# Kernel tuning notes

Measured on AMD Instinct MI355X. Metric: run time of the kernel, lower is better.

## Reference

```python
import jax, jax.numpy as jnp
import numpy as np

EMB = 768

def setup_inputs() -> dict:
    key = jax.random.key(0)
    ks = jax.random.split(key, 9)
    B, N, E = 8, 2048, EMB
    s = 1.0 / np.sqrt(E)
    return {
        "x":  jax.random.normal(ks[0], (B, N, E), jnp.float32),
        "Wq": jax.random.normal(ks[1], (E, E), jnp.float32) * s,
        "bq": jnp.zeros((E,), jnp.float32),
        "Wk": jax.random.normal(ks[2], (E, E), jnp.float32) * s,
        "bk": jnp.zeros((E,), jnp.float32),
        "Wv": jax.random.normal(ks[3], (E, E), jnp.float32) * s,
        "bv": jnp.zeros((E,), jnp.float32),
        "Wo": jax.random.normal(ks[4], (E, E), jnp.float32) * s,
        "bo": jnp.zeros((E,), jnp.float32),
    }

def reference(x, Wq, bq, Wk, bk, Wv, bv, Wo, bo):
    # Single-head attention; scale uses full emb dim (as in the source).
    E = x.shape[-1]
    q = jnp.einsum('bne,ef->bnf', x, Wq) + bq
    k = jnp.einsum('bne,ef->bnf', x, Wk) + bk
    v = jnp.einsum('bne,ef->bnf', x, Wv) + bv
    scores = jnp.einsum('bqe,bke->bqk', q, k) / jnp.sqrt(jnp.asarray(E, x.dtype))
    attn = jax.nn.softmax(scores, axis=-1)  # dropout is identity in eval mode
    out = jnp.einsum('bqk,bke->bqe', attn, v)
    return jnp.einsum('bne,ef->bnf', out, Wo) + bo
```

## Files before the change

### kernel.cpp

```cpp
#include <hip/hip_runtime.h>
#include <hip/hip_fp16.h>
#include <stdint.h>

typedef unsigned short u16;
typedef __attribute__((ext_vector_type(8))) __bf16 bf16x8;
typedef __attribute__((ext_vector_type(4))) float f32x4;

#define SEQ 2048
#define EMB 768
#define NB  8
#define LDQK (2 * EMB)

__device__ __forceinline__ u16 f2bf(float f) {
  union { float f; uint32_t u; } a; a.f = f;
  uint32_t r = a.u + 0x7fffu + ((a.u >> 16) & 1u);
  return (u16)(r >> 16);
}
__device__ __forceinline__ float bf2f(u16 h) {
  union { uint32_t u; float f; } a; a.u = ((uint32_t)h) << 16;
  return a.f;
}

__device__ __forceinline__ void swz_bid(int& bx, int& by, int& bz)
{
  const int gx = gridDim.x, gy = gridDim.y;
  const int nwg = gx * gy * gridDim.z;
  const int lid = ((int)blockIdx.z * gy + (int)blockIdx.y) * gx +
                  (int)blockIdx.x;
  const int cpx = nwg >> 3;
  const int orig = (lid & 7) * cpx + (lid >> 3);
  bx = orig % gx;
  const int t = orig / gx;
  by = t % gy;
  bz = t / gy;
}

__global__ __launch_bounds__(256) void k_detect_bias(
    const u16* __restrict__ x, int* __restrict__ flag,
    const void* __restrict__ b0, const void* __restrict__ b1,
    const void* __restrict__ b2, const void* __restrict__ b3,
    float* __restrict__ biasf)
{
  const int tid = threadIdx.x;
  int bad = 0;
#pragma unroll
  for (int i = 0; i < 4; ++i) {
    const u16 h = x[(tid * 4 + i) * 2];
    const int e = (h >> 7) & 0xFF;
    bad += (e >= 160 && e <= 254) ? 1 : 0;
  }
#pragma unroll
  for (int off = 32; off > 0; off >>= 1) bad += __shfl_down(bad, off);
  __shared__ int cnt[4];
  __shared__ int sflag;
  if ((tid & 63) == 0) cnt[tid >> 6] = bad;
  __syncthreads();
  if (tid == 0) {
    const int f = (cnt[0] + cnt[1] + cnt[2] + cnt[3] > 200) ? 1 : 0;
    sflag = f;
    *flag = f;
  }
  __syncthreads();
  const int f32 = sflag;
#pragma unroll
  for (int z = 0; z < 4; ++z) {
    const void* src = (z == 0) ? b0 : (z == 1) ? b1 : (z == 2) ? b2 : b3;
#pragma unroll
    for (int i = 0; i < 3; ++i) {
      const int j = tid + i * 256;
      biasf[z * EMB + j] = f32 ? ((const float*)src)[j]
                               : bf2f(((const u16*)src)[j]);
    }
  }
}

__global__ __launch_bounds__(256) void k_convert_x(
    const void* __restrict__ src, u16* __restrict__ dst,
    const int* __restrict__ flag, int n4)
{
  const int i = blockIdx.x * 256 + threadIdx.x;
  if (i >= n4) return;
  if (*flag) {
    const float4 f = ((const float4*)src)[i];
    ushort4 o;
    o.x = f2bf(f.x); o.y = f2bf(f.y); o.z = f2bf(f.z); o.w = f2bf(f.w);
    ((ushort4*)dst)[i] = o;
  } else {
    ((ushort4*)dst)[i] = ((const ushort4*)src)[i];
  }
}

__global__ __launch_bounds__(256) void k_transpose_w(
    const void* __restrict__ W0, const void* __restrict__ W1,
    const void* __restrict__ W2, const void* __restrict__ W3,
    u16* __restrict__ WT, const int* __restrict__ flag)
{
  __shared__ u16 t[32][33];
  const int z = blockIdx.z;
  const void* in = (z == 0) ? W0 : (z == 1) ? W1 : (z == 2) ? W2 : W3;
  u16* out = WT + (size_t)z * EMB * EMB;
  const int c0 = blockIdx.x * 32, r0 = blockIdx.y * 32;
  const int tx = threadIdx.x, ty = threadIdx.y;
  const int f32 = *flag;
#pragma unroll
  for (int i = 0; i < 4; ++i) {
    const size_t idx = (size_t)(r0 + ty + i * 8) * EMB + c0 + tx;
    t[ty + i * 8][tx] = f32 ? f2bf(((const float*)in)[idx])
                            : ((const u16*)in)[idx];
  }
  __syncthreads();
#pragma unroll
  for (int i = 0; i < 4; ++i)
    out[(size_t)(c0 + ty + i * 8) * EMB + r0 + tx] = t[tx][ty + i * 8];
}

template <int EPI>
__device__ __forceinline__ void gemm_core(
    const u16* __restrict__ A, int lda,
    const u16* __restrict__ BT, int ldbt,
    void* __restrict__ Cp, int ldc,
    const float* __restrict__ biasf, const int* __restrict__ of32,
    float scale, int K, int m0, int n0)
{
  __shared__ __align__(16) u16 As[128 * 64];
  __shared__ __align__(16) u16 Bs[128 * 64];
  const int tid  = threadIdx.x;
  const int lane = tid & 63;
  const int wave = tid >> 6;
  const int wr   = (wave >> 1) * 64;
  const int wc   = (wave & 1) * 64;
  const int lrow = lane & 15;
  const int quad = lane >> 4;

  f32x4 acc[4][4];
#pragma unroll
  for (int i = 0; i < 4; ++i)
#pragma unroll
    for (int j = 0; j < 4; ++j)
#pragma unroll
      for (int r = 0; r < 4; ++r) acc[i][j][r] = 0.0f;

  for (int kt = 0; kt < K; kt += 64) {
#pragma unroll
    for (int i = 0; i < 4; ++i) {
      const int c = wave * 256 + i * 64 + lane;
      const int r = c >> 3, s = c & 7;
      const int ss = s ^ (r & 7);
      const u16* ga = A  + (size_t)(m0 + r) * lda  + kt + ss * 8;
      const u16* gb = BT + (size_t)(n0 + r) * ldbt + kt + ss * 8;
      u16* la = As + (size_t)(wave * 256 + i * 64) * 8;
      u16* lb = Bs + (size_t)(wave * 256 + i * 64) * 8;
      __builtin_amdgcn_global_load_lds(
          (const __attribute__((address_space(1))) void*)ga,
          (__attribute__((address_space(3))) void*)la, 16, 0, 0);
      __builtin_amdgcn_global_load_lds(
          (const __attribute__((address_space(1))) void*)gb,
          (__attribute__((address_space(3))) void*)lb, 16, 0, 0);
    }
    __syncthreads();

#pragma unroll
    for (int kk = 0; kk < 2; ++kk) {
      bf16x8 af[4], bfr[4];
#pragma unroll
      for (int i = 0; i < 4; ++i) {
        const int row = wr + i * 16 + lrow;
        const int cs  = ((kk << 2) + quad) ^ (lrow & 7);
        af[i] = *(const bf16x8*)(As + row * 64 + cs * 8);
      }
#pragma unroll
      for (int j = 0; j < 4; ++j) {
        const int row = wc + j * 16 + lrow;
        const int cs  = ((kk << 2) + quad) ^ (lrow & 7);
        bfr[j] = *(const bf16x8*)(Bs + row * 64 + cs * 8);
      }
#pragma unroll
      for (int i = 0; i < 4; ++i)
#pragma unroll
        for (int j = 0; j < 4; ++j)
          acc[i][j] = __builtin_amdgcn_mfma_f32_16x16x32_bf16(
              af[i], bfr[j], acc[i][j], 0, 0, 0);
    }
    __syncthreads();
  }

  if (EPI == 3) {
    u16* C = (u16*)Cp;
#pragma unroll
    for (int i = 0; i < 4; ++i)
#pragma unroll
      for (int j = 0; j < 4; ++j)
#pragma unroll
        for (int r = 0; r < 4; ++r) {
          const int row = m0 + wr + i * 16 + quad * 4 + r;
          const int col = n0 + wc + j * 16 + lrow;
          C[(size_t)row * ldc + col] =
              __half_as_ushort(__float2half(acc[i][j][r] * scale));
        }
  } else if (EPI == 2) {
    u16* C = (u16*)Cp;
#pragma unroll
    for (int i = 0; i < 4; ++i)
#pragma unroll
      for (int j = 0; j < 4; ++j)
#pragma unroll
        for (int r = 0; r < 4; ++r) {
          const int row = m0 + wr + i * 16 + quad * 4 + r;
          const int col = n0 + wc + j * 16 + lrow;
          C[(size_t)row * ldc + col] = f2bf(acc[i][j][r]);
        }
  } else if (EPI == 5) {
    u16* C = (u16*)Cp;
#pragma unroll
    for (int i = 0; i < 4; ++i)
#pragma unroll
      for (int r = 0; r < 4; ++r) {
        const int row = m0 + wr + i * 16 + quad * 4 + r;
        const float bv = biasf[row];
#pragma unroll
        for (int j = 0; j < 4; ++j) {
          const int col = n0 + wc + j * 16 + lrow;
          C[(size_t)row * ldc + col] = f2bf(acc[i][j][r] + bv);
        }
      }
  } else {
    float bv[4];
#pragma unroll
    for (int j = 0; j < 4; ++j) bv[j] = biasf[n0 + wc + j * 16 + lrow];
    const bool f32out = (of32 != nullptr) && (*of32 != 0);
    if (f32out) {
      float* C = (float*)Cp;
#pragma unroll
      for (int i = 0; i < 4; ++i)
#pragma unroll
        for (int j = 0; j < 4; ++j)
#pragma unroll
          for (int r = 0; r < 4; ++r) {
            const int row = m0 + wr + i * 16 + quad * 4 + r;
            const int col = n0 + wc + j * 16 + lrow;
            C[(size_t)row * ldc + col] = acc[i][j][r] + bv[j];
          }
    } else {
      u16* C = (u16*)Cp;
#pragma unroll
      for (int i = 0; i < 4; ++i)
#pragma unroll
        for (int j = 0; j < 4; ++j)
#pragma unroll
          for (int r = 0; r < 4; ++r) {
            const int row = m0 + wr + i * 16 + quad * 4 + r;
            const int col = n0 + wc + j * 16 + lrow;
            C[(size_t)row * ldc + col] = f2bf(acc[i][j][r] + bv[j]);
          }
    }
  }
}


__global__ __launch_bounds__(256) void k_gemm_qk(
    const u16* __restrict__ A, const u16* __restrict__ BT,
    u16* __restrict__ QK, const float* __restrict__ biasf)
{
  int bx, by, bz; swz_bid(bx, by, bz);
  gemm_core<0>(A, EMB, BT, EMB, QK, LDQK, biasf, nullptr, 1.0f, EMB,
               by * 128, bx * 128);
}

__global__ __launch_bounds__(256) void k_gemm_vt(
    const u16* __restrict__ WvT, const u16* __restrict__ xb,
    u16* __restrict__ VT, const float* __restrict__ biasv)
{
  int bx, by, bz; swz_bid(bx, by, bz);
  const int b = bz;
  gemm_core<5>(WvT, EMB,
               xb + (size_t)b * SEQ * EMB, EMB,
               VT + (size_t)b * EMB * SEQ, SEQ,
               biasv, nullptr, 1.0f, EMB,
               by * 128, bx * 128);
}

__global__ __launch_bounds__(256) void k_gemm_out(
    const u16* __restrict__ A, const u16* __restrict__ BT,
    void* __restrict__ C, const float* __restrict__ biasf,
    const int* __restrict__ of32)
{
  int bx, by, bz; swz_bid(bx, by, bz);
  gemm_core<0>(A, EMB, BT, EMB, C, EMB, biasf, of32, 1.0f, EMB,
               by * 128, bx * 128);
}

__global__ __launch_bounds__(256) void k_gemm_scores(
    const u16* __restrict__ QK, u16* __restrict__ S, int b0)
{
  int bx, by, bz; swz_bid(bx, by, bz);
  const int b = b0 + bz;
  const u16* base = QK + (size_t)b * SEQ * LDQK;
  gemm_core<3>(base, LDQK,
               base + EMB, LDQK,
               S + (size_t)bz * SEQ * SEQ, SEQ,
               nullptr, nullptr,
               0.03608439182435161f , EMB,
               by * 128, bx * 128);
}

__global__ __launch_bounds__(256) void k_gemm_pv(
    const u16* __restrict__ P, const u16* __restrict__ VT,
    u16* __restrict__ O, int b0)
{
  int bx, by, bz; swz_bid(bx, by, bz);
  const int b = b0 + bz;
  gemm_core<2>(P  + (size_t)bz * SEQ * SEQ, SEQ,
               VT + (size_t)b * EMB * SEQ, SEQ,
               O  + (size_t)b * SEQ * EMB, EMB,
               nullptr, nullptr, 1.0f, SEQ,
               by * 128, bx * 128);
}

__global__ __launch_bounds__(256) void k_softmax(u16* __restrict__ S)
{
  u16* row = S + ((size_t)blockIdx.y * SEQ + blockIdx.x) * SEQ;
  const int tid = threadIdx.x;

  uint4 raw = *(const uint4*)(row + tid * 8);
  const u16* h = (const u16*)&raw;
  float v[8];
#pragma unroll
  for (int i = 0; i < 8; ++i) v[i] = __half2float(__ushort_as_half(h[i]));

  float mx = v[0];
#pragma unroll
  for (int i = 1; i < 8; ++i) mx = fmaxf(mx, v[i]);
#pragma unroll
  for (int off = 32; off > 0; off >>= 1) mx = fmaxf(mx, __shfl_down(mx, off));
  __shared__ float red[4], red2[4];
  if ((tid & 63) == 0) red[tid >> 6] = mx;
  __syncthreads();
  mx = fmaxf(fmaxf(red[0], red[1]), fmaxf(red[2], red[3]));

  float s = 0.0f;
#pragma unroll
  for (int i = 0; i < 8; ++i) { v[i] = __expf(v[i] - mx); s += v[i]; }
#pragma unroll
  for (int off = 32; off > 0; off >>= 1) s += __shfl_down(s, off);
  if ((tid & 63) == 0) red2[tid >> 6] = s;
  __syncthreads();
  s = red2[0] + red2[1] + red2[2] + red2[3];
  const float inv = 1.0f / s;

  uint4 outv;
  u16* o = (u16*)&outv;
#pragma unroll
  for (int i = 0; i < 8; ++i) o[i] = f2bf(v[i] * inv);
  *(uint4*)(row + tid * 8) = outv;
}


extern "C" void kernel_launch(void* const* d_in, const int* in_sizes, int n_in,
                              void* d_out, int out_size, void* d_ws, size_t ws_size,
                              hipStream_t stream)
{
  (void)in_sizes; (void)n_in; (void)out_size;
  const void* x  = d_in[0];
  const void* Wq = d_in[1];
  const void* bq = d_in[2];
  const void* Wk = d_in[3];
  const void* bk = d_in[4];
  const void* Wv = d_in[5];
  const void* bv = d_in[6];
  const void* Wo = d_in[7];
  const void* bo = d_in[8];

  char* ws = (char*)d_ws;
  size_t off = 0;
  auto alloc = [&](size_t bytes) -> void* {
    void* p = ws + off;
    off += (bytes + 255) & ~(size_t)255;
    return p;
  };
  int*   flag  = (int*)alloc(256);
  u16*   xb    = (u16*)alloc((size_t)NB * SEQ * EMB * 2);
  u16*   QK    = (u16*)alloc((size_t)NB * SEQ * LDQK * 2);
  u16*   VT    = (u16*)alloc((size_t)NB * EMB * SEQ * 2);
  u16*   O     = (u16*)alloc((size_t)NB * SEQ * EMB * 2);
  u16*   WT    = (u16*)alloc((size_t)4 * EMB * EMB * 2);
  float* biasf = (float*)alloc((size_t)4 * EMB * 4);
  u16*   S     = (u16*)(ws + off);
  size_t rem   = (ws_size > off) ? ws_size - off : 0;

  int GB = 8;
  while (GB > 1 && (size_t)GB * ((size_t)SEQ * SEQ * 2) > rem) GB >>= 1;

  k_detect_bias<<<1, 256, 0, stream>>>((const u16*)x, flag, bq, bk, bv, bo,
                                       biasf);
  const int n4 = NB * SEQ * EMB / 4;
  k_convert_x<<<(n4 + 255) / 256, 256, 0, stream>>>(x, xb, flag, n4);
  k_transpose_w<<<dim3(EMB / 32, EMB / 32, 4), dim3(32, 8), 0, stream>>>(
      Wq, Wk, Wv, Wo, WT, flag);

  k_gemm_qk<<<dim3(12, 128), 256, 0, stream>>>(xb, WT, QK, biasf);
  k_gemm_vt<<<dim3(16, 6, NB), 256, 0, stream>>>(
      WT + (size_t)2 * EMB * EMB, xb, VT, biasf + 2 * EMB);

  for (int g = 0; g < NB; g += GB) {
    k_gemm_scores<<<dim3(16, 16, GB), 256, 0, stream>>>(QK, S, g);
    k_softmax<<<dim3(SEQ, GB), 256, 0, stream>>>(S);
    k_gemm_pv<<<dim3(6, 16, GB), 256, 0, stream>>>(S, VT, O, g);
  }

  k_gemm_out<<<dim3(6, 128), 256, 0, stream>>>(O, WT + 3 * EMB * EMB, d_out,
                                               biasf + 3 * EMB, flag);
}
```

Before: 402.4 us.

## Replace GEMM core with 256x256 double-buffered, 8-wave pipelined MFMA kernel

```diff
diff --git a/kernel.cpp b/kernel.cpp
--- a/kernel.cpp
+++ b/kernel.cpp
@@ -10,6 +10,13 @@
 #define EMB 768
 #define NB  8
 #define LDQK (2 * EMB)
+
+#define VMCNT(n) asm volatile("s_waitcnt vmcnt(" #n ")" ::: "memory")
+#define LGKM(n)                                            \
+  do {                                                     \
+    asm volatile("s_waitcnt lgkmcnt(" #n ")" ::: "memory"); \
+    __builtin_amdgcn_sched_barrier(0);                     \
+  } while (0)
 
 __device__ __forceinline__ u16 f2bf(float f) {
   union { float f; uint32_t u; } a; a.f = f;
@@ -114,206 +121,270 @@
     out[(size_t)(c0 + ty + i * 8) * EMB + r0 + tx] = t[tx][ty + i * 8];
 }
 
+template <int NLO>
+__device__ __forceinline__ void mfma_grp(f32x4 (&acc)[8][4],
+                                         const bf16x8 (&Afr)[8],
+                                         const bf16x8 (&Bfr)[4])
+{
+#pragma unroll
+  for (int m = 0; m < 8; ++m) {
+    acc[m][NLO] = __builtin_amdgcn_mfma_f32_16x16x32_bf16(
+        Afr[m], Bfr[NLO], acc[m][NLO], 0, 0, 0);
+    acc[m][NLO + 1] = __builtin_amdgcn_mfma_f32_16x16x32_bf16(
+        Afr[m], Bfr[NLO + 1], acc[m][NLO + 1], 0, 0, 0);
+  }
+}
+
 template <int EPI>
-__device__ __forceinline__ void gemm_core(
+__device__ __forceinline__ void gemm_core256(
     const u16* __restrict__ A, int lda,
     const u16* __restrict__ BT, int ldbt,
     void* __restrict__ Cp, int ldc,
     const float* __restrict__ biasf, const int* __restrict__ of32,
     float scale, int K, int m0, int n0)
 {
-  __shared__ __align__(16) u16 As[128 * 64];
-  __shared__ __align__(16) u16 Bs[128 * 64];
+  __shared__ __align__(16) u16 LDSU[65536];
   const int tid  = threadIdx.x;
   const int lane = tid & 63;
   const int wave = tid >> 6;
-  const int wr   = (wave >> 1) * 64;
-  const int wc   = (wave & 1) * 64;
+  const int wm   = wave >> 2;
+  const int wn   = wave & 3;
   const int lrow = lane & 15;
   const int quad = lane >> 4;
-
-  f32x4 acc[4][4];
-#pragma unroll
-  for (int i = 0; i < 4; ++i)
-#pragma unroll
-    for (int j = 0; j < 4; ++j)
-#pragma unroll
-      for (int r = 0; r < 4; ++r) acc[i][j][r] = 0.0f;
-
-  for (int kt = 0; kt < K; kt += 64) {
-#pragma unroll
-    for (int i = 0; i < 4; ++i) {
-      const int c = wave * 256 + i * 64 + lane;
-      const int r = c >> 3, s = c & 7;
-      const int ss = s ^ (r & 7);
-      const u16* ga = A  + (size_t)(m0 + r) * lda  + kt + ss * 8;
-      const u16* gb = BT + (size_t)(n0 + r) * ldbt + kt + ss * 8;
-      u16* la = As + (size_t)(wave * 256 + i * 64) * 8;
-      u16* lb = Bs + (size_t)(wave * 256 + i * 64) * 8;
+  const int NT   = K >> 6;
+
+  auto STAGE = [&](const u16* __restrict__ G, int ld, int org, int t,
+                   int mat, int kh) {
+    const int buf = t & 1;
+#pragma unroll
+    for (int i = 0; i < 2; ++i) {
+      const int c   = i * 512 + tid;
+      const int row = c >> 2;
+      const int ss4 = (c & 3) ^ ((row >> 1) & 3);
+      const u16* g = G + (size_t)(org + row) * ld + t * 64 + kh * 32 + ss4 * 8;
+      u16* l = LDSU + buf * 32768 + mat * 16384 + kh * 8192 + (c & ~63) * 8;
       __builtin_amdgcn_global_load_lds(
-          (const __attribute__((address_space(1))) void*)ga,
-          (__attribute__((address_space(3))) void*)la, 16, 0, 0);
-      __builtin_amdgcn_global_load_lds(
-          (const __attribute__((address_space(1))) void*)gb,
-          (__attribute__((address_space(3))) void*)lb, 16, 0, 0);
+          (const __attribute__((address_space(1))) void*)g,
+          (__attribute__((address_space(3))) void*)l, 16, 0, 0);
     }
-    __syncthreads();
-
-#pragma unroll
-    for (int kk = 0; kk < 2; ++kk) {
-      bf16x8 af[4], bfr[4];
-#pragma unroll
-      for (int i = 0; i < 4; ++i) {
-        const int row = wr + i * 16 + lrow;
-        const int cs  = ((kk << 2) + quad) ^ (lrow & 7);
-        af[i] = *(const bf16x8*)(As + row * 64 + cs * 8);
-      }
-#pragma unroll
-      for (int j = 0; j < 4; ++j) {
-        const int row = wc + j * 16 + lrow;
-        const int cs  = ((kk << 2) + quad) ^ (lrow & 7);
-        bfr[j] = *(const bf16x8*)(Bs + row * 64 + cs * 8);
-      }
-#pragma unroll
-      for (int i = 0; i < 4; ++i)
-#pragma unroll
-        for (int j = 0; j < 4; ++j)
-          acc[i][j] = __builtin_amdgcn_mfma_f32_16x16x32_bf16(
-              af[i], bfr[j], acc[i][j], 0, 0, 0);
+  };
+
+  auto FRAG = [&](int t, int mat, int kh, int row) -> bf16x8 {
+    const int buf = t & 1;
+    const u16* p = LDSU + buf * 32768 + mat * 16384 + kh * 8192 + row * 32 +
+                   ((quad ^ ((row >> 1) & 3)) * 8);
+    bf16x8 r;
+    asm volatile("ds_read_b128 %0, %1"
+                 : "=v"(r)
+                 : "v"((const __attribute__((address_space(3))) u16*)p));
+    return r;
+  };
+
+  f32x4 acc[8][4];
+#pragma unroll
+  for (int m = 0; m < 8; ++m)
+#pragma unroll
+    for (int n = 0; n < 4; ++n)
+#pragma unroll
+      for (int r = 0; r < 4; ++r) acc[m][n][r] = 0.0f;
+
+  bf16x8 Af0[8], Af1[8], Bf0[4], Bf1[4];
+
+  const int arow = wm * 128 + lrow;
+  const int brow = wn * 64 + lrow;
+
+  STAGE(A, lda, m0, 0, 0, 0); STAGE(BT, ldbt, n0, 0, 1, 0);
+  STAGE(A, lda, m0, 0, 0, 1); STAGE(BT, ldbt, n0, 0, 1, 1);
+  STAGE(A, lda, m0, 1, 0, 0); STAGE(BT, ldbt, n0, 1, 1, 0);
+  STAGE(A, lda, m0, 1, 0, 1); STAGE(BT, ldbt, n0, 1, 1, 1);
+  VMCNT(8);
+  __builtin_amdgcn_s_barrier();
+#pragma unroll
+  for (int m = 0; m < 8; ++m) Af0[m] = FRAG(0, 0, 0, arow + m * 16);
+  Bf0[0] = FRAG(0, 1, 0, brow);
+  Bf0[1] = FRAG(0, 1, 0, brow + 16);
+
+  for (int u = 0; u < NT; ++u) {
+    const bool s2 = (u + 2) < NT;
+    Bf0[2] = FRAG(u, 1, 0, brow + 32);
+    Bf0[3] = FRAG(u, 1, 0, brow + 48);
+    if (s2) STAGE(A, lda, m0, u + 2, 0, 0);
+    __builtin_amdgcn_s_barrier();
+    LGKM(2);
+    __builtin_amdgcn_s_setprio(1);
+    mfma_grp<0>(acc, Af0, Bf0);
+    __builtin_amdgcn_s_setprio(0);
+    __builtin_amdgcn_s_barrier();
+#pragma unroll
+    for (int m = 0; m < 8; ++m) Af1[m] = FRAG(u, 0, 1, arow + m * 16);
+    Bf1[0] = FRAG(u, 1, 1, brow);
+    Bf1[1] = FRAG(u, 1, 1, brow + 16);
+    if (s2) STAGE(BT, ldbt, n0, u + 2, 1, 0);
+    __builtin_amdgcn_s_barrier();
+    LGKM(10);
+    __builtin_amdgcn_s_setprio(1);
+    mfma_grp<2>(acc, Af0, Bf0);
+    __builtin_amdgcn_s_setprio(0);
+    __builtin_amdgcn_s_barrier();
+    Bf1[2] = FRAG(u, 1, 1, brow + 32);
+    Bf1[3] = FRAG(u, 1, 1, brow + 48);
+    if (s2) STAGE(A, lda, m0, u + 2, 0, 1);
+    __builtin_amdgcn_s_barrier();
+    LGKM(2);
+    __builtin_amdgcn_s_setprio(1);
+    mfma_grp<0>(acc, Af1, Bf1);
+    __builtin_amdgcn_s_setprio(0);
+    __builtin_amdgcn_s_barrier();
+    if (s2) { VMCNT(6); } else { VMCNT(0); }
+    if (s2) STAGE(BT, ldbt, n0, u + 2, 1, 1);
+    __builtin_amdgcn_s_barrier();
+    if (u + 1 < NT) {
+#pragma unroll
+      for (int m = 0; m < 8; ++m) Af0[m] = FRAG(u + 1, 0, 0, arow + m * 16);
+      Bf0[0] = FRAG(u + 1, 1, 0, brow);
+      Bf0[1] = FRAG(u + 1, 1, 0, brow + 16);
+      LGKM(10);
+    } else {
+      LGKM(0);
     }
-    __syncthreads();
-  }
-
+    __builtin_amdgcn_s_setprio(1);
+    mfma_grp<2>(acc, Af1, Bf1);
+    __builtin_amdgcn_s_setprio(0);
+    __builtin_amdgcn_s_barrier();
+  }
+
+  const int rb = m0 + wm * 128 + quad * 4;
+  const int cb = n0 + wn * 64 + lrow;
   if (EPI == 3) {
     u16* C = (u16*)Cp;
 #pragma unroll
-    for (int i = 0; i < 4; ++i)
-#pragma unroll
-      for (int j = 0; j < 4; ++j)
+    for (int m = 0; m < 8; ++m)
+#pragma unroll
+      for (int n = 0; n < 4; ++n)
 #pragma unroll
         for (int r = 0; r < 4; ++r) {
-          const int row = m0 + wr + i * 16 + quad * 4 + r;
-          const int col = n0 + wc + j * 16 + lrow;
+          const int row = rb + m * 16 + r;
+          const int col = cb + n * 16;
           C[(size_t)row * ldc + col] =
-              __half_as_ushort(__float2half(acc[i][j][r] * scale));
+              __half_as_ushort(__float2half(acc[m][n][r] * scale));
         }
   } else if (EPI == 2) {
     u16* C = (u16*)Cp;
 #pragma unroll
-    for (int i = 0; i < 4; ++i)
-#pragma unroll
-      for (int j = 0; j < 4; ++j)
+    for (int m = 0; m < 8; ++m)
+#pragma unroll
+      for (int n = 0; n < 4; ++n)
 #pragma unroll
         for (int r = 0; r < 4; ++r) {
-          const int row = m0 + wr + i * 16 + quad * 4 + r;
-          const int col = n0 + wc + j * 16 + lrow;
-          C[(size_t)row * ldc + col] = f2bf(acc[i][j][r]);
+          const int row = rb + m * 16 + r;
+          const int col = cb + n * 16;
+          C[(size_t)row * ldc + col] = f2bf(acc[m][n][r]);
         }
   } else if (EPI == 5) {
     u16* C = (u16*)Cp;
 #pragma unroll
-    for (int i = 0; i < 4; ++i)
+    for (int m = 0; m < 8; ++m)
 #pragma unroll
       for (int r = 0; r < 4; ++r) {
-        const int row = m0 + wr + i * 16 + quad * 4 + r;
+        const int row = rb + m * 16 + r;
         const float bv = biasf[row];
 #pragma unroll
-        for (int j = 0; j < 4; ++j) {
-          const int col = n0 + wc + j * 16 + lrow;
-          C[(size_t)row * ldc + col] = f2bf(acc[i][j][r] + bv);
+        for (int n = 0; n < 4; ++n) {
+          const int col = cb + n * 16;
+          C[(size_t)row * ldc + col] = f2bf(acc[m][n][r] + bv);
         }
       }
   } else {
     float bv[4];
 #pragma unroll
-    for (int j = 0; j < 4; ++j) bv[j] = biasf[n0 + wc + j * 16 + lrow];
+    for (int n = 0; n < 4; ++n) bv[n] = biasf[cb + n * 16];
     const bool f32out = (of32 != nullptr) && (*of32 != 0);
     if (f32out) {
       float* C = (float*)Cp;
 #pragma unroll
-      for (int i = 0; i < 4; ++i)
-#pragma unroll
-        for (int j = 0; j < 4; ++j)
+      for (int m = 0; m < 8; ++m)
+#pragma unroll
+        for (int n = 0; n < 4; ++n)
 #pragma unroll
           for (int r = 0; r < 4; ++r) {
-            const int row = m0 + wr + i * 16 + quad * 4 + r;
-            const int col = n0 + wc + j * 16 + lrow;
-            C[(size_t)row * ldc + col] = acc[i][j][r] + bv[j];
+            const int row = rb + m * 16 + r;
+            const int col = cb + n * 16;
+            C[(size_t)row * ldc + col] = acc[m][n][r] + bv[n];
           }
     } else {
       u16* C = (u16*)Cp;
 #pragma unroll
-      for (int i = 0; i < 4; ++i)
-#pragma unroll
-        for (int j = 0; j < 4; ++j)
+      for (int m = 0; m < 8; ++m)
+#pragma unroll
+        for (int n = 0; n < 4; ++n)
 #pragma unroll
           for (int r = 0; r < 4; ++r) {
-            const int row = m0 + wr + i * 16 + quad * 4 + r;
-            const int col = n0 + wc + j * 16 + lrow;
-            C[(size_t)row * ldc + col] = f2bf(acc[i][j][r] + bv[j]);
+            const int row = rb + m * 16 + r;
+            const int col = cb + n * 16;
+            C[(size_t)row * ldc + col] = f2bf(acc[m][n][r] + bv[n]);
           }
     }
   }
 }
 
 
-__global__ __launch_bounds__(256) void k_gemm_qk(
+__global__ __launch_bounds__(512) void k_gemm_qk(
     const u16* __restrict__ A, const u16* __restrict__ BT,
     u16* __restrict__ QK, const float* __restrict__ biasf)
 {
   int bx, by, bz; swz_bid(bx, by, bz);
-  gemm_core<0>(A, EMB, BT, EMB, QK, LDQK, biasf, nullptr, 1.0f, EMB,
-               by * 128, bx * 128);
-}
-
-__global__ __launch_bounds__(256) void k_gemm_vt(
+  gemm_core256<0>(A, EMB, BT, EMB, QK, LDQK, biasf, nullptr, 1.0f, EMB,
+                  by * 256, bx * 256);
+}
+
+__global__ __launch_bounds__(512) void k_gemm_vt(
     const u16* __restrict__ WvT, const u16* __restrict__ xb,
     u16* __restrict__ VT, const float* __restrict__ biasv)
 {
   int bx, by, bz; swz_bid(bx, by, bz);
   const int b = bz;
-  gemm_core<5>(WvT, EMB,
-               xb + (size_t)b * SEQ * EMB, EMB,
-               VT + (size_t)b * EMB * SEQ, SEQ,
-               biasv, nullptr, 1.0f, EMB,
-               by * 128, bx * 128);
-}
-
-__global__ __launch_bounds__(256) void k_gemm_out(
+  gemm_core256<5>(WvT, EMB,
+                  xb + (size_t)b * SEQ * EMB, EMB,
+                  VT + (size_t)b * EMB * SEQ, SEQ,
+                  biasv, nullptr, 1.0f, EMB,
+                  by * 256, bx * 256);
+}
+
+__global__ __launch_bounds__(512) void k_gemm_out(
     const u16* __restrict__ A, const u16* __restrict__ BT,
     void* __restrict__ C, const float* __restrict__ biasf,
     const int* __restrict__ of32)
 {
   int bx, by, bz; swz_bid(bx, by, bz);
-  gemm_core<0>(A, EMB, BT, EMB, C, EMB, biasf, of32, 1.0f, EMB,
-               by * 128, bx * 128);
-}
-
-__global__ __launch_bounds__(256) void k_gemm_scores(
+  gemm_core256<0>(A, EMB, BT, EMB, C, EMB, biasf, of32, 1.0f, EMB,
+                  by * 256, bx * 256);
+}
+
+__global__ __launch_bounds__(512) void k_gemm_scores(
     const u16* __restrict__ QK, u16* __restrict__ S, int b0)
 {
   int bx, by, bz; swz_bid(bx, by, bz);
   const int b = b0 + bz;
   const u16* base = QK + (size_t)b * SEQ * LDQK;
-  gemm_core<3>(base, LDQK,
-               base + EMB, LDQK,
-               S + (size_t)bz * SEQ * SEQ, SEQ,
-               nullptr, nullptr,
-               0.03608439182435161f , EMB,
-               by * 128, bx * 128);
-}
-
-__global__ __launch_bounds__(256) void k_gemm_pv(
+  gemm_core256<3>(base, LDQK,
+                  base + EMB, LDQK,
+                  S + (size_t)bz * SEQ * SEQ, SEQ,
+                  nullptr, nullptr,
+                  0.03608439182435161f , EMB,
+                  by * 256, bx * 256);
+}
+
+__global__ __launch_bounds__(512) void k_gemm_pv(
     const u16* __restrict__ P, const u16* __restrict__ VT,
     u16* __restrict__ O, int b0)
 {
   int bx, by, bz; swz_bid(bx, by, bz);
   const int b = b0 + bz;
-  gemm_core<2>(P  + (size_t)bz * SEQ * SEQ, SEQ,
-               VT + (size_t)b * EMB * SEQ, SEQ,
-               O  + (size_t)b * SEQ * EMB, EMB,
-               nullptr, nullptr, 1.0f, SEQ,
-               by * 128, bx * 128);
+  gemm_core256<2>(P  + (size_t)bz * SEQ * SEQ, SEQ,
+                  VT + (size_t)b * EMB * SEQ, SEQ,
+                  O  + (size_t)b * SEQ * EMB, EMB,
+                  nullptr, nullptr, 1.0f, SEQ,
+                  by * 256, bx * 256);
 }
 
 __global__ __launch_bounds__(256) void k_softmax(u16* __restrict__ S)
@@ -397,16 +468,16 @@
   k_transpose_w<<<dim3(EMB / 32, EMB / 32, 4), dim3(32, 8), 0, stream>>>(
       Wq, Wk, Wv, Wo, WT, flag);
 
-  k_gemm_qk<<<dim3(12, 128), 256, 0, stream>>>(xb, WT, QK, biasf);
-  k_gemm_vt<<<dim3(16, 6, NB), 256, 0, stream>>>(
+  k_gemm_qk<<<dim3(6, 64), 512, 0, stream>>>(xb, WT, QK, biasf);
+  k_gemm_vt<<<dim3(8, 3, NB), 512, 0, stream>>>(
       WT + (size_t)2 * EMB * EMB, xb, VT, biasf + 2 * EMB);
 
   for (int g = 0; g < NB; g += GB) {
-    k_gemm_scores<<<dim3(16, 16, GB), 256, 0, stream>>>(QK, S, g);
+    k_gemm_scores<<<dim3(8, 8, GB), 512, 0, stream>>>(QK, S, g);
     k_softmax<<<dim3(SEQ, GB), 256, 0, stream>>>(S);
-    k_gemm_pv<<<dim3(6, 16, GB), 256, 0, stream>>>(S, VT, O, g);
-  }
-
-  k_gemm_out<<<dim3(6, 128), 256, 0, stream>>>(O, WT + 3 * EMB * EMB, d_out,
-                                               biasf + 3 * EMB, flag);
-}
+    k_gemm_pv<<<dim3(3, 8, GB), 512, 0, stream>>>(S, VT, O, g);
+  }
+
+  k_gemm_out<<<dim3(3, 64), 512, 0, stream>>>(O, WT + 3 * EMB * EMB, d_out,
+                                              biasf + 3 * EMB, flag);
+}
```

Measured after the change: 367.3 us. 1.1x faster.
